# Optimization experiments

Hardware: AMD Instinct MI355X
Metric: run time of the kernel (lower is better)

## Reference

```python
import jax, jax.numpy as jnp
import numpy as np

DICT = 24576  # SAE dictionary size
BATCH = 8192  # tokens per batch
K = 64        # active latents


def setup_inputs() -> dict:
    key = jax.random.key(0)
    z = jax.random.normal(key, (BATCH, DICT), dtype=jnp.float32)
    return {"z": z, "k": K}


def reference(z, k):
    # top-k along last dim, then scatter values back into a zero tensor
    vals, idx = jax.lax.top_k(z, k)            # [B, k]
    rows = jnp.arange(z.shape[0])[:, None]     # [B, 1] row indices for batched scatter
    out = jnp.zeros_like(z).at[rows, idx].set(vals)
    return out
```

## Files before the change

kernel.cpp:

```cpp
#include <hip/hip_runtime.h>
#include <stdint.h>

#define DICT  24576
#define BLOCK 1024
#define PER   24
#define NV    6
#define EQCAP 256

__device__ __forceinline__ uint32_t f2key(float f) {
    uint32_t u = __float_as_uint(f);
    return (u & 0x80000000u) ? ~u : (u | 0x80000000u);
}
__device__ __forceinline__ float key2f(uint32_t kk) {
    uint32_t u = (kk & 0x80000000u) ? (kk ^ 0x80000000u) : ~kk;
    return __uint_as_float(u);
}

template<int LO, int NBITS, bool FIRST>
__device__ __forceinline__ void radix_pass(const uint32_t (&key)[PER],
                                           uint32_t* hist,
                                           uint32_t* s_bstar,
                                           uint32_t* s_r,
                                           uint32_t& prefix, uint32_t& r,
                                           int tid) {
    constexpr int NB = 1 << NBITS;
    constexpr int PER_SEG = NB / 64;

    __syncthreads();
    for (int i = tid; i < NB; i += BLOCK) hist[i] = 0;
    __syncthreads();

    #pragma unroll
    for (int e = 0; e < PER; ++e) {
        uint32_t kk = key[e];
        bool part = FIRST ? true : ((kk >> (LO + NBITS)) == prefix);
        if (part) {
            uint32_t b = (kk >> LO) & (NB - 1);
            atomicAdd(&hist[b], 1u);
        }
    }
    __syncthreads();

    if (tid < 64) {
        uint32_t segsum = 0;
        #pragma unroll
        for (int i = 0; i < PER_SEG; ++i) {
            int idx = tid * PER_SEG + ((i + tid) & (PER_SEG - 1));
            segsum += hist[idx];
        }
        uint32_t S = segsum;
        #pragma unroll
        for (int off = 1; off < 64; off <<= 1) {
            uint32_t v = __shfl_down(S, off, 64);
            if (tid + off < 64) S += v;
        }
        uint32_t A = S - segsum;
        bool cross = (A < r) && (S >= r);
        unsigned long long m = __ballot(cross);
        int seg = __ffsll(m) - 1;
        uint32_t aboveSeg = __shfl(A, seg, 64);
        uint32_t h = 0;
        if (tid < PER_SEG) h = hist[seg * PER_SEG + tid];
        uint32_t S2 = h;
        #pragma unroll
        for (int off = 1; off < PER_SEG; off <<= 1) {
            uint32_t v = __shfl_down(S2, off, 64);
            if (tid + off < PER_SEG) S2 += v;
        }
        uint32_t A2 = aboveSeg + S2 - h;
        if (tid < PER_SEG && A2 < r && A2 + h >= r) {
            *s_bstar = (uint32_t)(seg * PER_SEG + tid);
            *s_r = r - A2;
        }
    }
    __syncthreads();
    prefix = (prefix << NBITS) | *s_bstar;
    r = *s_r;
}

__global__ __launch_bounds__(BLOCK) void topk_kernel(const float* __restrict__ z,
                                                     const int* __restrict__ kp,
                                                     float* __restrict__ out) {
    __shared__ uint32_t hist[2048];
    __shared__ uint32_t s_bstar, s_r, eqCount;
    __shared__ uint32_t eqIdx[EQCAP];

    const int tid = threadIdx.x;
    const int row = blockIdx.x;
    const uint32_t k = (uint32_t)kp[0];

    const float4* zr = (const float4*)(z + (size_t)row * DICT);
    float4* outr = (float4*)(out + (size_t)row * DICT);

    uint32_t key[PER];
    #pragma unroll
    for (int j = 0; j < NV; ++j) {
        float4 v = zr[j * BLOCK + tid];
        key[j*4+0] = f2key(v.x);
        key[j*4+1] = f2key(v.y);
        key[j*4+2] = f2key(v.z);
        key[j*4+3] = f2key(v.w);
    }

    uint32_t prefix = 0, r = k;
    radix_pass<21, 11, true >(key, hist, &s_bstar, &s_r, prefix, r, tid);
    radix_pass<10, 11, false>(key, hist, &s_bstar, &s_r, prefix, r, tid);
    radix_pass< 0, 10, false>(key, hist, &s_bstar, &s_r, prefix, r, tid);
    const uint32_t T = prefix;

    if (tid == 0) eqCount = 0;
    __syncthreads();
    #pragma unroll
    for (int e = 0; e < PER; ++e) {
        if (key[e] == T) {
            uint32_t slot = atomicAdd(&eqCount, 1u);
            if (slot < EQCAP) {
                int j = e >> 2, c = e & 3;
                eqIdx[slot] = (uint32_t)(j * 4096 + tid * 4 + c);
            }
        }
    }
    __syncthreads();
    const uint32_t ec = eqCount < EQCAP ? eqCount : EQCAP;

    #pragma unroll
    for (int j = 0; j < NV; ++j) {
        float vals[4];
        #pragma unroll
        for (int c = 0; c < 4; ++c) {
            uint32_t kk = key[j*4 + c];
            float val = 0.0f;
            if (kk > T) {
                val = key2f(kk);
            } else if (kk == T) {
                uint32_t gi = (uint32_t)(j * 4096 + tid * 4 + c);
                uint32_t rank = 0;
                for (uint32_t i = 0; i < ec; ++i) rank += (eqIdx[i] < gi) ? 1u : 0u;
                if (rank < r) val = key2f(kk);
            }
            vals[c] = val;
        }
        float4 o;
        o.x = vals[0]; o.y = vals[1]; o.z = vals[2]; o.w = vals[3];
        outr[j * BLOCK + tid] = o;
    }
}

extern "C" void kernel_launch(void* const* d_in, const int* in_sizes, int n_in,
                              void* d_out, int out_size, void* d_ws, size_t ws_size,
                              hipStream_t stream) {
    const float* z = (const float*)d_in[0];
    const int*   kp = (const int*)d_in[1];
    float* out = (float*)d_out;
    const int batch = in_sizes[0] / DICT;
    topk_kernel<<<dim3(batch), dim3(BLOCK), 0, stream>>>(z, kp, out);
}
```

Measured before the change: 1.360 ms.

## Restructure radix top-k with candidate compaction, replicated histograms, and input re-reads

Drops the 24-key register array and re-reads the row from global memory (likely L2-resident) on each pass, so more blocks can be resident per CU (launch bounds now request 8 blocks). The first pass uses four padded histogram copies to cut atomic contention. The second pass compacts the elements matching the first bucket into shared candidate lists, so the third pass and tie handling only scan those candidates. The tie-ranking path is skipped when there are no ties at the threshold. The costs are extra global reads and more shared memory, and a fallback full rescan is kept for when the candidate list overflows.

```diff
diff --git a/kernel.cpp b/kernel.cpp
--- a/kernel.cpp
+++ b/kernel.cpp
@@ -3,153 +3,205 @@
 
 #define DICT  24576
 #define BLOCK 1024
-#define PER   24
 #define NV    6
-#define EQCAP 256
+#define NB1   2048
+#define NB2   2048
+#define NB3   1024
+#define NCOPY 4
+#define HPAD  8
+#define HSTRIDE (NB1 + HPAD)
+#define CAND_CAP 3072
+#define EQCAP 1024
 
 __device__ __forceinline__ uint32_t f2key(float f) {
     uint32_t u = __float_as_uint(f);
     return (u & 0x80000000u) ? ~u : (u | 0x80000000u);
 }
-__device__ __forceinline__ float key2f(uint32_t kk) {
-    uint32_t u = (kk & 0x80000000u) ? (kk ^ 0x80000000u) : ~kk;
-    return __uint_as_float(u);
-}
-
-template<int LO, int NBITS, bool FIRST>
-__device__ __forceinline__ void radix_pass(const uint32_t (&key)[PER],
-                                           uint32_t* hist,
-                                           uint32_t* s_bstar,
-                                           uint32_t* s_r,
-                                           uint32_t& prefix, uint32_t& r,
-                                           int tid) {
-    constexpr int NB = 1 << NBITS;
+
+template<int NB>
+__device__ __forceinline__ void scan_hist(const uint32_t* __restrict__ hist,
+                                          uint32_t r, int lane,
+                                          uint32_t& bstar, uint32_t& rin,
+                                          uint32_t& hcnt) {
     constexpr int PER_SEG = NB / 64;
-
-    __syncthreads();
-    for (int i = tid; i < NB; i += BLOCK) hist[i] = 0;
-    __syncthreads();
-
-    #pragma unroll
-    for (int e = 0; e < PER; ++e) {
-        uint32_t kk = key[e];
-        bool part = FIRST ? true : ((kk >> (LO + NBITS)) == prefix);
-        if (part) {
-            uint32_t b = (kk >> LO) & (NB - 1);
-            atomicAdd(&hist[b], 1u);
-        }
-    }
-    __syncthreads();
-
-    if (tid < 64) {
-        uint32_t segsum = 0;
-        #pragma unroll
-        for (int i = 0; i < PER_SEG; ++i) {
-            int idx = tid * PER_SEG + ((i + tid) & (PER_SEG - 1));
-            segsum += hist[idx];
-        }
-        uint32_t S = segsum;
-        #pragma unroll
-        for (int off = 1; off < 64; off <<= 1) {
-            uint32_t v = __shfl_down(S, off, 64);
-            if (tid + off < 64) S += v;
-        }
-        uint32_t A = S - segsum;
-        bool cross = (A < r) && (S >= r);
-        unsigned long long m = __ballot(cross);
-        int seg = __ffsll(m) - 1;
-        uint32_t aboveSeg = __shfl(A, seg, 64);
-        uint32_t h = 0;
-        if (tid < PER_SEG) h = hist[seg * PER_SEG + tid];
-        uint32_t S2 = h;
-        #pragma unroll
-        for (int off = 1; off < PER_SEG; off <<= 1) {
-            uint32_t v = __shfl_down(S2, off, 64);
-            if (tid + off < PER_SEG) S2 += v;
-        }
-        uint32_t A2 = aboveSeg + S2 - h;
-        if (tid < PER_SEG && A2 < r && A2 + h >= r) {
-            *s_bstar = (uint32_t)(seg * PER_SEG + tid);
-            *s_r = r - A2;
-        }
-    }
-    __syncthreads();
-    prefix = (prefix << NBITS) | *s_bstar;
-    r = *s_r;
-}
-
-__global__ __launch_bounds__(BLOCK) void topk_kernel(const float* __restrict__ z,
-                                                     const int* __restrict__ kp,
-                                                     float* __restrict__ out) {
-    __shared__ uint32_t hist[2048];
-    __shared__ uint32_t s_bstar, s_r, eqCount;
+    uint32_t segsum = 0;
+    #pragma unroll
+    for (int i = 0; i < PER_SEG; ++i) {
+        int idx = lane * PER_SEG + ((i + lane) & (PER_SEG - 1));
+        segsum += hist[idx];
+    }
+    uint32_t S = segsum;
+    #pragma unroll
+    for (int off = 1; off < 64; off <<= 1) {
+        uint32_t v = __shfl_down(S, off, 64);
+        if (lane + off < 64) S += v;
+    }
+    uint32_t A = S - segsum;
+    unsigned long long m = __ballot((A < r) && (S >= r));
+    int seg = __ffsll(m) - 1;
+    uint32_t aboveSeg = __shfl(A, seg, 64);
+    uint32_t h = (lane < PER_SEG) ? hist[seg * PER_SEG + lane] : 0u;
+    uint32_t S2 = h;
+    #pragma unroll
+    for (int off = 1; off < PER_SEG; off <<= 1) {
+        uint32_t v = __shfl_down(S2, off, 64);
+        if (lane + off < PER_SEG) S2 += v;
+    }
+    uint32_t A2 = aboveSeg + S2 - h;
+    unsigned long long m2 = __ballot((lane < PER_SEG) && (A2 < r) && (A2 + h >= r));
+    int j = __ffsll(m2) - 1;
+    bstar = (uint32_t)(seg * PER_SEG + j);
+    rin   = r - __shfl(A2, j, 64);
+    hcnt  = __shfl(h, j, 64);
+}
+
+__global__ __launch_bounds__(BLOCK, 8)
+void topk_kernel(const float* __restrict__ z,
+                 const int* __restrict__ kp,
+                 float* __restrict__ out) {
+    __shared__ uint32_t hist[NCOPY * HSTRIDE];
+    __shared__ uint32_t candKey[CAND_CAP];
+    __shared__ uint32_t candIdx[CAND_CAP];
     __shared__ uint32_t eqIdx[EQCAP];
-
-    const int tid = threadIdx.x;
-    const int row = blockIdx.x;
+    __shared__ uint32_t candCount, eqCount;
+
+    const int tid  = threadIdx.x;
+    const int lane = tid & 63;
+    const int row  = blockIdx.x;
     const uint32_t k = (uint32_t)kp[0];
 
-    const float4* zr = (const float4*)(z + (size_t)row * DICT);
-    float4* outr = (float4*)(out + (size_t)row * DICT);
-
-    uint32_t key[PER];
+    const float4* __restrict__ zr  = (const float4*)(z + (size_t)row * DICT);
+    float4* __restrict__ outr = (float4*)(out + (size_t)row * DICT);
+
+    for (int i = tid; i < NCOPY * HSTRIDE; i += BLOCK) hist[i] = 0;
+    __syncthreads();
+    uint32_t* myh = hist + ((tid >> 6) & (NCOPY - 1)) * HSTRIDE;
+    #pragma unroll
+    for (int half = 0; half < 2; ++half) {
+        float4 v[3];
+        #pragma unroll
+        for (int j = 0; j < 3; ++j) v[j] = zr[(half * 3 + j) * BLOCK + tid];
+        #pragma unroll
+        for (int j = 0; j < 3; ++j) {
+            atomicAdd(&myh[f2key(v[j].x) >> 21], 1u);
+            atomicAdd(&myh[f2key(v[j].y) >> 21], 1u);
+            atomicAdd(&myh[f2key(v[j].z) >> 21], 1u);
+            atomicAdd(&myh[f2key(v[j].w) >> 21], 1u);
+        }
+    }
+    __syncthreads();
+    for (int i = tid; i < NB1; i += BLOCK)
+        hist[i] = hist[i] + hist[HSTRIDE + i] + hist[2 * HSTRIDE + i] + hist[3 * HSTRIDE + i];
+    __syncthreads();
+    uint32_t b1, r1, h1;
+    scan_hist<NB1>(hist, k, lane, b1, r1, h1);
+
+    __syncthreads();
+    for (int i = tid; i < NB2; i += BLOCK) hist[i] = 0;
+    if (tid == 0) { candCount = 0; eqCount = 0; }
+    __syncthreads();
     #pragma unroll
     for (int j = 0; j < NV; ++j) {
-        float4 v = zr[j * BLOCK + tid];
-        key[j*4+0] = f2key(v.x);
-        key[j*4+1] = f2key(v.y);
-        key[j*4+2] = f2key(v.z);
-        key[j*4+3] = f2key(v.w);
-    }
-
-    uint32_t prefix = 0, r = k;
-    radix_pass<21, 11, true >(key, hist, &s_bstar, &s_r, prefix, r, tid);
-    radix_pass<10, 11, false>(key, hist, &s_bstar, &s_r, prefix, r, tid);
-    radix_pass< 0, 10, false>(key, hist, &s_bstar, &s_r, prefix, r, tid);
-    const uint32_t T = prefix;
-
-    if (tid == 0) eqCount = 0;
-    __syncthreads();
-    #pragma unroll
-    for (int e = 0; e < PER; ++e) {
-        if (key[e] == T) {
-            uint32_t slot = atomicAdd(&eqCount, 1u);
-            if (slot < EQCAP) {
-                int j = e >> 2, c = e & 3;
-                eqIdx[slot] = (uint32_t)(j * 4096 + tid * 4 + c);
+        float4 vv = zr[j * BLOCK + tid];
+        uint32_t kk[4] = { f2key(vv.x), f2key(vv.y), f2key(vv.z), f2key(vv.w) };
+        #pragma unroll
+        for (int c = 0; c < 4; ++c) {
+            if ((kk[c] >> 21) == b1) {
+                atomicAdd(&hist[(kk[c] >> 10) & (NB2 - 1)], 1u);
+                uint32_t slot = atomicAdd(&candCount, 1u);
+                if (slot < CAND_CAP) {
+                    candKey[slot] = kk[c];
+                    candIdx[slot] = (uint32_t)(j * (BLOCK * 4) + tid * 4 + c);
+                }
             }
         }
     }
     __syncthreads();
-    const uint32_t ec = eqCount < EQCAP ? eqCount : EQCAP;
+    uint32_t b2, r2, h2;
+    scan_hist<NB2>(hist, r1, lane, b2, r2, h2);
+    const uint32_t pre22 = (b1 << 11) | b2;
+    const uint32_t nc = candCount;
+
+    __syncthreads();
+    for (int i = tid; i < NB3; i += BLOCK) hist[i] = 0;
+    __syncthreads();
+    if (nc <= CAND_CAP) {
+        for (uint32_t i = tid; i < nc; i += BLOCK) {
+            uint32_t kk = candKey[i];
+            if ((kk >> 10) == pre22) atomicAdd(&hist[kk & (NB3 - 1)], 1u);
+        }
+    } else {
+        #pragma unroll
+        for (int j = 0; j < NV; ++j) {
+            float4 vv = zr[j * BLOCK + tid];
+            uint32_t kk[4] = { f2key(vv.x), f2key(vv.y), f2key(vv.z), f2key(vv.w) };
+            #pragma unroll
+            for (int c = 0; c < 4; ++c)
+                if ((kk[c] >> 10) == pre22) atomicAdd(&hist[kk[c] & (NB3 - 1)], 1u);
+        }
+    }
+    __syncthreads();
+    uint32_t b3, r3, h3;
+    scan_hist<NB3>(hist, r2, lane, b3, r3, h3);
+    const uint32_t T = (pre22 << 10) | b3;
+
+    const bool needTies = (r3 < h3);
+    if (needTies) {
+        if (nc <= CAND_CAP) {
+            for (uint32_t i = tid; i < nc; i += BLOCK)
+                if (candKey[i] == T) {
+                    uint32_t s = atomicAdd(&eqCount, 1u);
+                    if (s < EQCAP) eqIdx[s] = candIdx[i];
+                }
+        } else {
+            #pragma unroll
+            for (int j = 0; j < NV; ++j) {
+                float4 vv = zr[j * BLOCK + tid];
+                uint32_t kk[4] = { f2key(vv.x), f2key(vv.y), f2key(vv.z), f2key(vv.w) };
+                #pragma unroll
+                for (int c = 0; c < 4; ++c)
+                    if (kk[c] == T) {
+                        uint32_t s = atomicAdd(&eqCount, 1u);
+                        if (s < EQCAP) eqIdx[s] = (uint32_t)(j * (BLOCK * 4) + tid * 4 + c);
+                    }
+            }
+        }
+        __syncthreads();
+    }
+    const uint32_t ec = needTies ? (eqCount < EQCAP ? eqCount : EQCAP) : 0u;
 
     #pragma unroll
     for (int j = 0; j < NV; ++j) {
-        float vals[4];
+        float4 vv = zr[j * BLOCK + tid];
+        float vals[4] = { vv.x, vv.y, vv.z, vv.w };
+        float o[4];
         #pragma unroll
         for (int c = 0; c < 4; ++c) {
-            uint32_t kk = key[j*4 + c];
+            uint32_t kk = f2key(vals[c]);
             float val = 0.0f;
             if (kk > T) {
-                val = key2f(kk);
+                val = vals[c];
             } else if (kk == T) {
-                uint32_t gi = (uint32_t)(j * 4096 + tid * 4 + c);
-                uint32_t rank = 0;
-                for (uint32_t i = 0; i < ec; ++i) rank += (eqIdx[i] < gi) ? 1u : 0u;
-                if (rank < r) val = key2f(kk);
+                if (!needTies) {
+                    val = vals[c];
+                } else {
+                    uint32_t gi = (uint32_t)(j * (BLOCK * 4) + tid * 4 + c);
+                    uint32_t rank = 0;
+                    for (uint32_t i = 0; i < ec; ++i) rank += (eqIdx[i] < gi) ? 1u : 0u;
+                    if (rank < r3) val = vals[c];
+                }
             }
-            vals[c] = val;
-        }
-        float4 o;
-        o.x = vals[0]; o.y = vals[1]; o.z = vals[2]; o.w = vals[3];
-        outr[j * BLOCK + tid] = o;
+            o[c] = val;
+        }
+        float4 ov; ov.x = o[0]; ov.y = o[1]; ov.z = o[2]; ov.w = o[3];
+        outr[j * BLOCK + tid] = ov;
     }
 }
 
 extern "C" void kernel_launch(void* const* d_in, const int* in_sizes, int n_in,
                               void* d_out, int out_size, void* d_ws, size_t ws_size,
                               hipStream_t stream) {
-    const float* z = (const float*)d_in[0];
+    const float* z  = (const float*)d_in[0];
     const int*   kp = (const int*)d_in[1];
     float* out = (float*)d_out;
     const int batch = in_sizes[0] / DICT;
```

Result: slower. 1.542 ms (+13.4%).
